# Kernel optimization log

Hardware: AMD Instinct MI355X
Metric: run time of the kernel (lower is better)

Reference implementation:

```python
import jax, jax.numpy as jnp
import numpy as np

NUM_EXPERTS = 64
TOP_K = 2
CAP_FACTOR = 1.0


def setup_inputs() -> dict:
    key = jax.random.key(0)
    k1, k2 = jax.random.split(key)
    x = jax.random.normal(k1, (8192, 4096), dtype=jnp.float32)
    wg = jax.random.normal(k2, (NUM_EXPERTS, 4096), dtype=jnp.float32) * 0.02
    return {"x": x, "wg": wg}


def reference(x, wg):
    # x: [S, M] tokens, wg: [E, M] gate weight (Linear, no bias)
    S, M = x.shape
    E, K = NUM_EXPERTS, TOP_K
    capacity = K * int(CAP_FACTOR * ((S + E - 1) // E))  # static

    logits = jnp.einsum('sm,em->se', x, wg)            # [S, E]
    gates = jax.nn.softmax(logits, axis=1)             # [S, E]
    _, topk_idx = jax.lax.top_k(logits, K)             # [S, K]

    masks = jax.nn.one_hot(topk_idx, E, dtype=x.dtype)  # [S, K, E]
    gates_s = jnp.einsum('se,ske->sk', gates, masks)    # [S, K]

    # load-balancing loss (fp32 path of load_balance)
    me = jnp.sum(gates, axis=0)                         # [E]
    ce = jnp.sum(masks[:, 0], axis=0)                   # [E]
    l_loss = jnp.sum(me * ce) * (E / (S * S))

    # capacity locations: cumsum-sub-one per k, offset by counts of earlier k's
    locs = jnp.cumsum(masks, axis=0) - 1.0              # [S, K, E]
    counts = jnp.sum(masks, axis=0)                     # [K, E]
    acc = jnp.concatenate([jnp.zeros((1, E), x.dtype),
                           jnp.cumsum(counts, axis=0)[:-1]], axis=0)  # [K, E]
    locs = locs + acc[None, :, :]
    loc_s = jnp.einsum('ske,ske->sk', locs, masks).astype(jnp.int32)  # [S, K]

    # postnorm gate normalization (top_k > 1)
    eps = jnp.finfo(gates_s.dtype).eps
    gates_n = gates_s / jnp.clip(jnp.sum(gates_s, axis=1, keepdims=True), eps)

    idx = topk_idx.astype(jnp.int32)                    # [S, K]
    valid = (loc_s >= 0) & (loc_s < capacity)           # [S, K]
    pos = jnp.where(valid, idx * capacity + loc_s, 0)   # [S, K] flat slot ids

    # encode: scatter tokens (unweighted, is_postnorm=True) into [E*capacity, M]
    contrib = jnp.where(valid[..., None], x[:, None, :], 0.0)  # [S, K, M]
    dispatched = jnp.zeros((E * capacity, M), x.dtype)
    dispatched = dispatched.at[pos.reshape(-1)].add(contrib.reshape(-1, M))

    # expert_fn = identity (world_size=1, routing pipeline is the op under test)
    expert_output = dispatched                          # [E*capacity, M]

    # decode: gather back and combine with normalized gates
    gathered = expert_output[pos.reshape(-1)].reshape(S, K, M)
    out = jnp.einsum('sk,skm->sm', gates_n * valid.astype(x.dtype), gathered)
    return out, l_loss
```

## Files before the change

### kernel.cpp

```cpp
#include <hip/hip_runtime.h>
#include <math.h>

#define S_TOK 8192
#define M_DIM 4096
#define NEXP 64
#define CAPACITY 256
#define NCHUNK 128
#define KS 8
#define KSL 512
#define BT 64
#define BK 32
#define NC (KSL / BK)

__global__ __launch_bounds__(256) void k_logits(
    const float* __restrict__ x, const float* __restrict__ wg,
    float* __restrict__ part)
{
    __shared__ float xs[2][BK * 64];
    __shared__ float wsl[2][BK * 64];
    const int tid = threadIdx.x;
    const int tile = blockIdx.x >> 3;
    const int ks   = blockIdx.x & 7;
    const int t0 = tile * BT;
    const int kb = ks * KSL;

    const int tx = tid & 15;
    const int ty = tid >> 4;

    float4 rx[2], rw[2];
    auto ld = [&](int kc) {
        #pragma unroll
        for (int i = 0; i < 2; ++i) {
            const int item = tid + 256 * i;
            const int r = item >> 3, kq = item & 7;
            rx[i] = *(const float4*)(x  + (size_t)(t0 + r) * M_DIM + kc + 4 * kq);
            rw[i] = *(const float4*)(wg + (size_t)r       * M_DIM + kc + 4 * kq);
        }
    };
    auto st = [&](int buf) {
        #pragma unroll
        for (int i = 0; i < 2; ++i) {
            const int item = tid + 256 * i;
            const int r = item >> 3, kq = item & 7;
            const int quad = r >> 2, lo = r & 3;
            const float vx[4] = {rx[i].x, rx[i].y, rx[i].z, rx[i].w};
            const float vw[4] = {rw[i].x, rw[i].y, rw[i].z, rw[i].w};
            #pragma unroll
            for (int j = 0; j < 4; ++j) {
                const int row = 4 * kq + j;
                const int addr = row * 64 + ((quad ^ kq) << 2) + lo;
                xs[buf][addr]  = vx[j];
                wsl[buf][addr] = vw[j];
            }
        }
    };

    float acc[4][4] = {};
    ld(kb);
    st(0);
    __syncthreads();
    for (int c = 0; c < NC; ++c) {
        const int buf = c & 1;
        if (c + 1 < NC) ld(kb + (c + 1) * BK);
        #pragma unroll 8
        for (int kk = 0; kk < BK; ++kk) {
            const int sw = kk >> 2;
            const float4 a = *(const float4*)&xs [buf][kk * 64 + ((ty ^ sw) << 2)];
            const float4 b = *(const float4*)&wsl[buf][kk * 64 + ((tx ^ sw) << 2)];
            const float av[4] = {a.x, a.y, a.z, a.w};
            const float bv[4] = {b.x, b.y, b.z, b.w};
            #pragma unroll
            for (int i = 0; i < 4; ++i)
                #pragma unroll
                for (int j = 0; j < 4; ++j)
                    acc[i][j] = fmaf(av[i], bv[j], acc[i][j]);
        }
        __syncthreads();
        if (c + 1 < NC) st(buf ^ 1);
        __syncthreads();
    }

    #pragma unroll
    for (int i = 0; i < 4; ++i) {
        float4 v;
        v.x = acc[i][0]; v.y = acc[i][1]; v.z = acc[i][2]; v.w = acc[i][3];
        *(float4*)(part + ((size_t)ks * S_TOK + t0 + 4 * ty + i) * NEXP + 4 * tx) = v;
    }
}

__global__ __launch_bounds__(256) void k_reduce(
    const float* __restrict__ part, float* __restrict__ me_g,
    int* __restrict__ idx0_g, int* __restrict__ idx1_g,
    float* __restrict__ gn0_g, float* __restrict__ gn1_g)
{
    __shared__ float me_sh[NEXP];
    const int tid = threadIdx.x;
    if (tid < NEXP) me_sh[tid] = 0.f;
    __syncthreads();

    const int wv = tid >> 6, lane = tid & 63;
    float me_acc = 0.f;
    for (int i = 0; i < 8; ++i) {
        const int t = blockIdx.x * 32 + wv * 8 + i;
        float lg = 0.f;
        #pragma unroll
        for (int s = 0; s < KS; ++s)
            lg += part[((size_t)s * S_TOK + t) * NEXP + lane];

        float v = lg; int id = lane;
        #pragma unroll
        for (int off = 32; off > 0; off >>= 1) {
            float v2 = __shfl_xor(v, off);
            int   i2 = __shfl_xor(id, off);
            if (v2 > v || (v2 == v && i2 < id)) { v = v2; id = i2; }
        }
        const float mx = v; const int i0 = id;

        const float p = expf(lg - mx);
        float sum = p;
        #pragma unroll
        for (int off = 32; off > 0; off >>= 1) sum += __shfl_xor(sum, off);
        me_acc += p / sum;

        float v1 = (lane == i0) ? -INFINITY : lg; int id1 = lane;
        #pragma unroll
        for (int off = 32; off > 0; off >>= 1) {
            float v2 = __shfl_xor(v1, off);
            int   i2 = __shfl_xor(id1, off);
            if (v2 > v1 || (v2 == v1 && i2 < id1)) { v1 = v2; id1 = i2; }
        }

        const float g0 = 1.0f / sum;
        const float g1 = expf(v1 - mx) / sum;
        const float den = fmaxf(g0 + g1, 1.1920929e-07f);
        if (lane == 0) {
            idx0_g[t] = i0;
            idx1_g[t] = id1;
            gn0_g[t] = g0 / den;
            gn1_g[t] = g1 / den;
        }
    }
    atomicAdd(&me_sh[lane], me_acc);
    __syncthreads();
    if (tid < NEXP) atomicAdd(&me_g[tid], me_sh[tid]);
}

__global__ __launch_bounds__(64) void k_rank(
    const int* __restrict__ idx0_g, const int* __restrict__ idx1_g,
    int* __restrict__ rank0_g, int* __restrict__ rank1_g,
    int* __restrict__ cnt_g )
{
    const int lane = threadIdx.x;
    const int chunk = blockIdx.x;
    const int s = chunk * 64 + lane;
    const int e0 = idx0_g[s], e1 = idx1_g[s];
    const unsigned long long lt = (1ull << lane) - 1ull;

    int r0 = 0, r1 = 0, c0 = 0, c1 = 0;
    #pragma unroll
    for (int e = 0; e < 64; ++e) {
        unsigned long long m0 = __ballot(e0 == e);
        unsigned long long m1 = __ballot(e1 == e);
        if (e0 == e) r0 = __popcll(m0 & lt);
        if (e1 == e) r1 = __popcll(m1 & lt);
        if (lane == e) { c0 = __popcll(m0); c1 = __popcll(m1); }
    }
    rank0_g[s] = r0;
    rank1_g[s] = r1;
    cnt_g[chunk * 64 + lane] = c0;
    cnt_g[NCHUNK * 64 + chunk * 64 + lane] = c1;
}

__global__ __launch_bounds__(256) void k_scan(
    const int* __restrict__ cnt_g, int* __restrict__ base_g,
    int* __restrict__ tot0_g, const float* __restrict__ me_g,
    float* __restrict__ loss_out)
{
    const int wv = threadIdx.x >> 6, lane = threadIdx.x & 63;
    const int g = blockIdx.x * 4 + wv;
    const int k = g >> 6, e = g & 63;

    const int c0 = cnt_g[(k * NCHUNK + 2 * lane)     * 64 + e];
    const int c1 = cnt_g[(k * NCHUNK + 2 * lane + 1) * 64 + e];
    const int s = c0 + c1;
    int incl = s;
    #pragma unroll
    for (int d = 1; d < 64; d <<= 1) {
        int v = __shfl_up(incl, d);
        if (lane >= d) incl += v;
    }
    const int excl = incl - s;
    base_g[(k * NCHUNK + 2 * lane)     * 64 + e] = excl;
    base_g[(k * NCHUNK + 2 * lane + 1) * 64 + e] = excl + c0;
    const int total = __shfl(incl, 63);
    if (k == 0 && lane == 0) {
        tot0_g[e] = total;
        atomicAdd(loss_out, me_g[e] * (float)total * 9.5367431640625e-07f);
    }
}

__global__ __launch_bounds__(256) void k_weight(
    const int* __restrict__ idx0_g, const int* __restrict__ idx1_g,
    const float* __restrict__ gn0_g, const float* __restrict__ gn1_g,
    const int* __restrict__ rank0_g, const int* __restrict__ rank1_g,
    const int* __restrict__ base_g, const int* __restrict__ tot0_g,
    float* __restrict__ w_g)
{
    const int s = blockIdx.x * 256 + threadIdx.x;
    const int chunk = s >> 6;
    const int e0 = idx0_g[s], e1 = idx1_g[s];
    const int loc0 = base_g[chunk * 64 + e0] + rank0_g[s];
    const int loc1 = base_g[(NCHUNK + chunk) * 64 + e1] + rank1_g[s] + tot0_g[e1];
    float w = 0.f;
    if (loc0 < CAPACITY) w += gn0_g[s];
    if (loc1 < CAPACITY) w += gn1_g[s];
    w_g[s] = w;
}

__global__ __launch_bounds__(256) void k_out(
    const float* __restrict__ x, const float* __restrict__ w_g,
    float* __restrict__ out)
{
    const int s = blockIdx.x;
    const float w = w_g[s];
    const float4* xr = (const float4*)(x + (size_t)s * M_DIM);
    float4* o = (float4*)(out + (size_t)s * M_DIM);
    #pragma unroll
    for (int i = 0; i < 4; ++i) {
        float4 v = xr[threadIdx.x + 256 * i];
        v.x *= w; v.y *= w; v.z *= w; v.w *= w;
        o[threadIdx.x + 256 * i] = v;
    }
}

extern "C" void kernel_launch(void* const* d_in, const int* in_sizes, int n_in,
                              void* d_out, int out_size, void* d_ws, size_t ws_size,
                              hipStream_t stream)
{
    const float* x  = (const float*)d_in[0];
    const float* wg = (const float*)d_in[1];
    float* out = (float*)d_out;
    float* loss = out + (size_t)S_TOK * M_DIM;

    float* part = (float*)d_ws;
    float* me   = part + (size_t)KS * S_TOK * NEXP;
    int*  idx0  = (int*)(me + NEXP);
    int*  idx1  = idx0 + S_TOK;
    float* gn0  = (float*)(idx1 + S_TOK);
    float* gn1  = gn0 + S_TOK;
    int*  rank0 = (int*)(gn1 + S_TOK);
    int*  rank1 = rank0 + S_TOK;
    int*  cnt   = rank1 + S_TOK;
    int*  base  = cnt + 2 * NCHUNK * 64;
    int*  tot0  = base + 2 * NCHUNK * 64;
    float* wtok = (float*)(tot0 + NEXP);

    hipMemsetAsync(me, 0, NEXP * sizeof(float), stream);
    hipMemsetAsync(loss, 0, sizeof(float), stream);

    k_logits<<<128 * KS, 256, 0, stream>>>(x, wg, part);
    k_reduce<<<S_TOK / 32, 256, 0, stream>>>(part, me, idx0, idx1, gn0, gn1);
    k_rank<<<NCHUNK, 64, 0, stream>>>(idx0, idx1, rank0, rank1, cnt);
    k_scan<<<32, 256, 0, stream>>>(cnt, base, tot0, me, loss);
    k_weight<<<S_TOK / 256, 256, 0, stream>>>(idx0, idx1, gn0, gn1,
                                              rank0, rank1, base, tot0, wtok);
    k_out<<<S_TOK, 256, 0, stream>>>(x, wtok, out);
}
```

Baseline: 313.5 us.

## Retile gate GEMM to 256-token 8x8 tiles and fuse routing kernels

The logits GEMM now uses 256-token tiles with an 8x8 per-thread register tile and a 16-way K split, in place of 64-token tiles with 4x4 per-thread tiles and an 8-way split. This raises FMA work per shared-memory load. The trade-off is twice as many partial-logit buffers to write and then read back in the reduction, and a larger workspace footprint. The reduce and rank kernels are merged into one 512-thread gate kernel that passes expert ids through shared memory. The per-token weight computation is folded into the output scaling kernel, which removes two launches and the intermediate weight buffer.

```diff
diff --git a/kernel.cpp b/kernel.cpp
--- a/kernel.cpp
+++ b/kernel.cpp
@@ -6,9 +6,9 @@
 #define NEXP 64
 #define CAPACITY 256
 #define NCHUNK 128
-#define KS 8
-#define KSL 512
-#define BT 64
+#define KS 16
+#define KSL 256
+#define BT 256
 #define BK 32
 #define NC (KSL / BK)
 
@@ -16,63 +16,75 @@
     const float* __restrict__ x, const float* __restrict__ wg,
     float* __restrict__ part)
 {
-    __shared__ float xs[2][BK * 64];
+    __shared__ float xs[2][BK * BT];
     __shared__ float wsl[2][BK * 64];
     const int tid = threadIdx.x;
-    const int tile = blockIdx.x >> 3;
-    const int ks   = blockIdx.x & 7;
+    const int tile = blockIdx.x >> 4;
+    const int ks   = blockIdx.x & 15;
     const int t0 = tile * BT;
     const int kb = ks * KSL;
 
-    const int tx = tid & 15;
-    const int ty = tid >> 4;
-
-    float4 rx[2], rw[2];
+    const int tx = tid & 7;
+    const int ty = tid >> 3;
+
+    float4 rx[8], rw[2];
     auto ld = [&](int kc) {
         #pragma unroll
+        for (int i = 0; i < 8; ++i) {
+            const int item = tid + 256 * i;
+            const int r = item >> 3, kq = item & 7;
+            rx[i] = *(const float4*)(x + (size_t)(t0 + r) * M_DIM + kc + 4 * kq);
+        }
+        #pragma unroll
         for (int i = 0; i < 2; ++i) {
             const int item = tid + 256 * i;
             const int r = item >> 3, kq = item & 7;
-            rx[i] = *(const float4*)(x  + (size_t)(t0 + r) * M_DIM + kc + 4 * kq);
-            rw[i] = *(const float4*)(wg + (size_t)r       * M_DIM + kc + 4 * kq);
+            rw[i] = *(const float4*)(wg + (size_t)r * M_DIM + kc + 4 * kq);
         }
     };
     auto st = [&](int buf) {
         #pragma unroll
+        for (int i = 0; i < 8; ++i) {
+            const int item = tid + 256 * i;
+            const int r = item >> 3, kq = item & 7;
+            const int quad = r >> 2, lo = r & 3;
+            const float v[4] = {rx[i].x, rx[i].y, rx[i].z, rx[i].w};
+            #pragma unroll
+            for (int j = 0; j < 4; ++j)
+                xs[buf][(4 * kq + j) * BT + ((quad ^ kq) << 2) + lo] = v[j];
+        }
+        #pragma unroll
         for (int i = 0; i < 2; ++i) {
             const int item = tid + 256 * i;
             const int r = item >> 3, kq = item & 7;
             const int quad = r >> 2, lo = r & 3;
-            const float vx[4] = {rx[i].x, rx[i].y, rx[i].z, rx[i].w};
-            const float vw[4] = {rw[i].x, rw[i].y, rw[i].z, rw[i].w};
+            const float v[4] = {rw[i].x, rw[i].y, rw[i].z, rw[i].w};
             #pragma unroll
-            for (int j = 0; j < 4; ++j) {
-                const int row = 4 * kq + j;
-                const int addr = row * 64 + ((quad ^ kq) << 2) + lo;
-                xs[buf][addr]  = vx[j];
-                wsl[buf][addr] = vw[j];
-            }
+            for (int j = 0; j < 4; ++j)
+                wsl[buf][(4 * kq + j) * 64 + ((quad ^ kq) << 2) + lo] = v[j];
         }
     };
 
-    float acc[4][4] = {};
+    float acc[8][8] = {};
     ld(kb);
     st(0);
     __syncthreads();
     for (int c = 0; c < NC; ++c) {
         const int buf = c & 1;
         if (c + 1 < NC) ld(kb + (c + 1) * BK);
-        #pragma unroll 8
+        #pragma unroll 4
         for (int kk = 0; kk < BK; ++kk) {
             const int sw = kk >> 2;
-            const float4 a = *(const float4*)&xs [buf][kk * 64 + ((ty ^ sw) << 2)];
-            const float4 b = *(const float4*)&wsl[buf][kk * 64 + ((tx ^ sw) << 2)];
-            const float av[4] = {a.x, a.y, a.z, a.w};
-            const float bv[4] = {b.x, b.y, b.z, b.w};
+            const float4 a0 = *(const float4*)&xs [buf][kk * BT + (((2 * ty)     ^ sw) << 2)];
+            const float4 a1 = *(const float4*)&xs [buf][kk * BT + (((2 * ty + 1) ^ sw) << 2)];
+            const float4 b0 = *(const float4*)&wsl[buf][kk * 64 + (((2 * tx)     ^ sw) << 2)];
+            const float4 b1 = *(const float4*)&wsl[buf][kk * 64 + (((2 * tx + 1) ^ sw) << 2)];
+            const float av[8] = {a0.x, a0.y, a0.z, a0.w, a1.x, a1.y, a1.z, a1.w};
+            const float bv[8] = {b0.x, b0.y, b0.z, b0.w, b1.x, b1.y, b1.z, b1.w};
             #pragma unroll
-            for (int i = 0; i < 4; ++i)
+            for (int i = 0; i < 8; ++i)
                 #pragma unroll
-                for (int j = 0; j < 4; ++j)
+                for (int j = 0; j < 8; ++j)
                     acc[i][j] = fmaf(av[i], bv[j], acc[i][j]);
         }
         __syncthreads();
@@ -81,27 +93,35 @@
     }
 
     #pragma unroll
-    for (int i = 0; i < 4; ++i) {
-        float4 v;
-        v.x = acc[i][0]; v.y = acc[i][1]; v.z = acc[i][2]; v.w = acc[i][3];
-        *(float4*)(part + ((size_t)ks * S_TOK + t0 + 4 * ty + i) * NEXP + 4 * tx) = v;
-    }
-}
-
-__global__ __launch_bounds__(256) void k_reduce(
+    for (int i = 0; i < 8; ++i) {
+        float4 v0, v1;
+        v0.x = acc[i][0]; v0.y = acc[i][1]; v0.z = acc[i][2]; v0.w = acc[i][3];
+        v1.x = acc[i][4]; v1.y = acc[i][5]; v1.z = acc[i][6]; v1.w = acc[i][7];
+        float* dst = part + ((size_t)ks * S_TOK + t0 + 8 * ty + i) * NEXP + 8 * tx;
+        *(float4*)dst = v0;
+        *(float4*)(dst + 4) = v1;
+    }
+}
+
+__global__ __launch_bounds__(512) void k_gate(
     const float* __restrict__ part, float* __restrict__ me_g,
     int* __restrict__ idx0_g, int* __restrict__ idx1_g,
-    float* __restrict__ gn0_g, float* __restrict__ gn1_g)
+    float* __restrict__ gn0_g, float* __restrict__ gn1_g,
+    int* __restrict__ rank0_g, int* __restrict__ rank1_g,
+    int* __restrict__ cnt_g )
 {
     __shared__ float me_sh[NEXP];
+    __shared__ int e0_sh[64], e1_sh[64];
     const int tid = threadIdx.x;
     if (tid < NEXP) me_sh[tid] = 0.f;
     __syncthreads();
 
     const int wv = tid >> 6, lane = tid & 63;
+    const int chunk = blockIdx.x;
     float me_acc = 0.f;
     for (int i = 0; i < 8; ++i) {
-        const int t = blockIdx.x * 32 + wv * 8 + i;
+        const int tt = wv * 8 + i;
+        const int t = chunk * 64 + tt;
         float lg = 0.f;
         #pragma unroll
         for (int s = 0; s < KS; ++s)
@@ -138,37 +158,32 @@
             idx1_g[t] = id1;
             gn0_g[t] = g0 / den;
             gn1_g[t] = g1 / den;
+            e0_sh[tt] = i0;
+            e1_sh[tt] = id1;
         }
     }
     atomicAdd(&me_sh[lane], me_acc);
     __syncthreads();
     if (tid < NEXP) atomicAdd(&me_g[tid], me_sh[tid]);
-}
-
-__global__ __launch_bounds__(64) void k_rank(
-    const int* __restrict__ idx0_g, const int* __restrict__ idx1_g,
-    int* __restrict__ rank0_g, int* __restrict__ rank1_g,
-    int* __restrict__ cnt_g )
-{
-    const int lane = threadIdx.x;
-    const int chunk = blockIdx.x;
-    const int s = chunk * 64 + lane;
-    const int e0 = idx0_g[s], e1 = idx1_g[s];
-    const unsigned long long lt = (1ull << lane) - 1ull;
-
-    int r0 = 0, r1 = 0, c0 = 0, c1 = 0;
-    #pragma unroll
-    for (int e = 0; e < 64; ++e) {
-        unsigned long long m0 = __ballot(e0 == e);
-        unsigned long long m1 = __ballot(e1 == e);
-        if (e0 == e) r0 = __popcll(m0 & lt);
-        if (e1 == e) r1 = __popcll(m1 & lt);
-        if (lane == e) { c0 = __popcll(m0); c1 = __popcll(m1); }
-    }
-    rank0_g[s] = r0;
-    rank1_g[s] = r1;
-    cnt_g[chunk * 64 + lane] = c0;
-    cnt_g[NCHUNK * 64 + chunk * 64 + lane] = c1;
+
+    if (wv == 0) {
+        const int s = chunk * 64 + lane;
+        const int e0 = e0_sh[lane], e1 = e1_sh[lane];
+        const unsigned long long lt = (1ull << lane) - 1ull;
+        int r0 = 0, r1 = 0, c0 = 0, c1 = 0;
+        #pragma unroll
+        for (int e = 0; e < 64; ++e) {
+            unsigned long long m0 = __ballot(e0 == e);
+            unsigned long long m1 = __ballot(e1 == e);
+            if (e0 == e) r0 = __popcll(m0 & lt);
+            if (e1 == e) r1 = __popcll(m1 & lt);
+            if (lane == e) { c0 = __popcll(m0); c1 = __popcll(m1); }
+        }
+        rank0_g[s] = r0;
+        rank1_g[s] = r1;
+        cnt_g[chunk * 64 + lane] = c0;
+        cnt_g[NCHUNK * 64 + chunk * 64 + lane] = c1;
+    }
 }
 
 __global__ __launch_bounds__(256) void k_scan(
@@ -199,14 +214,15 @@
     }
 }
 
-__global__ __launch_bounds__(256) void k_weight(
+__global__ __launch_bounds__(256) void k_out(
+    const float* __restrict__ x,
     const int* __restrict__ idx0_g, const int* __restrict__ idx1_g,
     const float* __restrict__ gn0_g, const float* __restrict__ gn1_g,
     const int* __restrict__ rank0_g, const int* __restrict__ rank1_g,
     const int* __restrict__ base_g, const int* __restrict__ tot0_g,
-    float* __restrict__ w_g)
-{
-    const int s = blockIdx.x * 256 + threadIdx.x;
+    float* __restrict__ out)
+{
+    const int s = blockIdx.x;
     const int chunk = s >> 6;
     const int e0 = idx0_g[s], e1 = idx1_g[s];
     const int loc0 = base_g[chunk * 64 + e0] + rank0_g[s];
@@ -214,15 +230,7 @@
     float w = 0.f;
     if (loc0 < CAPACITY) w += gn0_g[s];
     if (loc1 < CAPACITY) w += gn1_g[s];
-    w_g[s] = w;
-}
-
-__global__ __launch_bounds__(256) void k_out(
-    const float* __restrict__ x, const float* __restrict__ w_g,
-    float* __restrict__ out)
-{
-    const int s = blockIdx.x;
-    const float w = w_g[s];
+
     const float4* xr = (const float4*)(x + (size_t)s * M_DIM);
     float4* o = (float4*)(out + (size_t)s * M_DIM);
     #pragma unroll
@@ -253,16 +261,14 @@
     int*  cnt   = rank1 + S_TOK;
     int*  base  = cnt + 2 * NCHUNK * 64;
     int*  tot0  = base + 2 * NCHUNK * 64;
-    float* wtok = (float*)(tot0 + NEXP);
 
     hipMemsetAsync(me, 0, NEXP * sizeof(float), stream);
     hipMemsetAsync(loss, 0, sizeof(float), stream);
 
-    k_logits<<<128 * KS, 256, 0, stream>>>(x, wg, part);
-    k_reduce<<<S_TOK / 32, 256, 0, stream>>>(part, me, idx0, idx1, gn0, gn1);
-    k_rank<<<NCHUNK, 64, 0, stream>>>(idx0, idx1, rank0, rank1, cnt);
+    k_logits<<<32 * KS, 256, 0, stream>>>(x, wg, part);
+    k_gate<<<NCHUNK, 512, 0, stream>>>(part, me, idx0, idx1, gn0, gn1,
+                                       rank0, rank1, cnt);
     k_scan<<<32, 256, 0, stream>>>(cnt, base, tot0, me, loss);
-    k_weight<<<S_TOK / 256, 256, 0, stream>>>(idx0, idx1, gn0, gn1,
-                                              rank0, rank1, base, tot0, wtok);
-    k_out<<<S_TOK, 256, 0, stream>>>(x, wtok, out);
-}
+    k_out<<<S_TOK, 256, 0, stream>>>(x, idx0, idx1, gn0, gn1,
+                                     rank0, rank1, base, tot0, out);
+}
```

After: 308.5 us. Within noise of the previous version (-1.6%).
